# Optimization experiments

Hardware: AMD Instinct MI355X
Metric: run time of the kernel (lower is better)

The kernel has to match this reference:

```python
import jax, jax.numpy as jnp
import numpy as np
from jax import lax

NPOINT, RADIUS, NSAMPLE = 1024, 0.2, 32
MLP = [64, 64, 128]
EPS = 1e-5  # BatchNorm eps


def setup_inputs() -> dict:
    key = jax.random.key(0)
    ks = jax.random.split(key, 16)
    B, N, D = 16, 4096, 64
    inp = {
        "xyz": jax.random.uniform(ks[0], (B, 3, N), jnp.float32),   # points in unit cube
        "points": jax.random.normal(ks[1], (B, D, N), jnp.float32),  # per-point features
    }
    chans = [3 + D] + MLP  # grouped_xyz_norm (3) concat features (D)
    for i in range(3):
        ci, co = chans[i], chans[i + 1]
        inp[f"W{i}"] = jax.random.normal(ks[2 + 4 * i], (co, ci), jnp.float32) * (1.0 / np.sqrt(ci))
        inp[f"b{i}"] = jnp.zeros((co,), jnp.float32)
        inp[f"g{i}"] = jnp.ones((co,), jnp.float32)    # BN gamma
        inp[f"be{i}"] = jnp.zeros((co,), jnp.float32)  # BN beta
    return inp


def _fps(xyz, npoint):
    # xyz: [B,N,3] -> sampled indices [B,npoint]. Sequential farthest-point sampling.
    B, N, _ = xyz.shape

    def step(carry, _):
        distance, farthest = carry
        centroid = jnp.take_along_axis(xyz, farthest[:, None, None], axis=1)  # [B,1,3]
        d = jnp.sum((xyz - centroid) ** 2, -1)                                # [B,N]
        distance = jnp.minimum(distance, d)
        return (distance, jnp.argmax(distance, -1)), farthest

    init = (jnp.full((B, N), 1e10, xyz.dtype), jnp.zeros((B,), jnp.int32))
    _, idx = lax.scan(step, init, None, length=npoint)
    return idx.T  # [B, npoint]


def _index_points(pts, idx):
    # pts [B,N,C], idx [B,...] int -> [B,...,C]  (batched gather)
    return jax.vmap(lambda p, i: p[i])(pts, idx)


def _ball_query(radius, nsample, xyz, new_xyz):
    # xyz [B,N,3], new_xyz [B,S,3] -> group_idx [B,S,nsample]
    B, N, _ = xyz.shape
    sqr = (jnp.sum(new_xyz ** 2, -1)[:, :, None]
           + jnp.sum(xyz ** 2, -1)[:, None, :]
           - 2.0 * jnp.einsum('bsc,bnc->bsn', new_xyz, xyz))  # [B,S,N]
    # NB: source assigns N-1 (not N) to out-of-radius points; the == N fixup is a no-op,
    # kept here for faithfulness.
    gi = jnp.where(sqr > radius ** 2, N - 1, jnp.arange(N, dtype=jnp.int32)[None, None, :])
    gi = jnp.sort(gi, axis=-1)[:, :, :nsample]
    first = gi[:, :, :1]
    return jnp.where(gi == N, first, gi)


def _forward(xyz, points, params):
    xyzT = jnp.transpose(xyz, (0, 2, 1))    # [B,N,3]
    ptsT = jnp.transpose(points, (0, 2, 1))  # [B,N,D]
    B, N, _ = xyzT.shape
    fps_idx = _fps(xyzT, NPOINT)                              # [B,S]
    new_xyz = _index_points(xyzT, fps_idx)                    # [B,S,3]
    idx = _ball_query(RADIUS, NSAMPLE, xyzT, new_xyz)         # [B,S,K]
    grouped_xyz = _index_points(xyzT, idx) - new_xyz[:, :, None, :]  # [B,S,K,3]
    grouped_pts = _index_points(ptsT, idx)                    # [B,S,K,D]
    feat = jnp.concatenate([grouped_xyz, grouped_pts], -1)    # [B,S,K,3+D]
    x = jnp.transpose(feat, (0, 3, 2, 1))                     # [B,C,K,S]
    for (W, b, g, be) in params:
        x = jnp.einsum('bcks,oc->boks', x, W) + b[None, :, None, None]  # 1x1 conv
        mean = jnp.mean(x, axis=(0, 2, 3), keepdims=True)   # BN (training-mode batch stats)
        var = jnp.var(x, axis=(0, 2, 3), keepdims=True)
        x = (x - mean) / jnp.sqrt(var + EPS) * g[None, :, None, None] + be[None, :, None, None]
        x = jax.nn.relu(x)
    new_points = jnp.max(x, axis=2)                           # [B, mlp[-1], S]
    return jnp.transpose(new_xyz, (0, 2, 1)), new_points


def reference(xyz, points, W0, b0, g0, be0, W1, b1, g1, be1, W2, b2, g2, be2):
    params = [(W0, b0, g0, be0), (W1, b1, g1, be1), (W2, b2, g2, be2)]
    return _forward(xyz, points, params)
```

## Files before the change

### kernel.cpp

```cpp
#include <hip/hip_runtime.h>
#include <cstdint>
#include <cstddef>

#define BB 16
#define NN 4096
#define SS 1024
#define KK 32
#define MROWS (BB*SS*KK)
#define EPSV 1e-5f
#define OUT_OFF1 (BB*3*SS)

static constexpr size_t OFF_XYZT   = 0;
static constexpr size_t OFF_NEWXYZ = OFF_XYZT   + (size_t)BB*NN*16;
static constexpr size_t OFF_BALL   = OFF_NEWXYZ + (size_t)BB*SS*16;
static constexpr size_t OFF_STATS  = OFF_BALL   + (size_t)MROWS*4;
static constexpr size_t OFF_PROG   = OFF_STATS  + 2048;
static constexpr size_t OFF_PT     = OFF_PROG   + 256;
static constexpr size_t OFF_Y      = OFF_PT     + (size_t)BB*NN*64*4;
static constexpr size_t OFF_YMAX   = OFF_Y      + (size_t)MROWS*64*4;
static constexpr size_t OFF_YMIN   = OFF_YMAX   + (size_t)BB*SS*128*4;

__device__ __forceinline__ float sq3(float x, float y, float z) {
  return __fadd_rn(__fadd_rn(__fmul_rn(x,x), __fmul_rn(y,y)), __fmul_rn(z,z));
}

template<int CTRL>
__device__ __forceinline__ unsigned long long dpp_max_u64(unsigned long long k) {
  int lo = (int)(unsigned)k;
  int hi = (int)(unsigned)(k >> 32);
  unsigned olo = (unsigned)__builtin_amdgcn_update_dpp(0, lo, CTRL, 0xf, 0xf, true);
  unsigned ohi = (unsigned)__builtin_amdgcn_update_dpp(0, hi, CTRL, 0xf, 0xf, true);
  unsigned long long o = ((unsigned long long)ohi << 32) | (unsigned long long)olo;
  return o > k ? o : k;
}

__global__ __launch_bounds__(256) void trans_kernel(const float* __restrict__ xyz,
                                                    const float* __restrict__ pts,
                                                    float4* __restrict__ xyzt,
                                                    float* __restrict__ pt) {
  __shared__ float tl[64*65];
  int t = threadIdx.x;
  int k = blockIdx.x;
  int b = k >> 6, n0 = (k & 63) * 64;
  int ln = t & 63, hi = t >> 6;
#pragma unroll
  for (int i = 0; i < 16; ++i) {
    int c = 4*i + hi;
    tl[c*65 + ln] = pts[((size_t)b*64 + c)*NN + n0 + ln];
  }
  if (t < 64) {
    int n = n0 + t;
    const float* xb = xyz + (size_t)b*3*NN;
    xyzt[(size_t)b*NN + n] = make_float4(xb[n], xb[NN+n], xb[2*NN+n], 0.f);
  }
  __syncthreads();
#pragma unroll
  for (int i = 0; i < 16; ++i) {
    int nn = hi + 4*i;
    pt[((size_t)b*NN + n0 + nn)*64 + ln] = tl[ln*65 + nn];
  }
}

__global__ __launch_bounds__(256) void fps_ball_conv0(const float* __restrict__ xyz,
                                                      const float4* __restrict__ xyzt,
                                                      const float* __restrict__ pt,
                                                      float4* __restrict__ newxyz,
                                                      int* __restrict__ prog,
                                                      float* __restrict__ out,
                                                      const float* __restrict__ W0,
                                                      const float* __restrict__ bias0,
                                                      float* __restrict__ y,
                                                      float* __restrict__ stats0) {
  __shared__ __align__(16) char smem[65600];
  int t = threadIdx.x;

  if (blockIdx.x >= 16) {
    float4* Ws4  = (float4*)smem;
    float*  Ws   = (float*)Ws4;
    float4* Xs4  = (float4*)(smem + 17408);
    int*    bidx = (int*)(smem + 52224);
    int lane = t & 63, wv = t >> 6;
    int base = (blockIdx.x - 16)*4;
    int bs = base + wv;
    int b = bs >> 10;

    for (int idx = t; idx < 68*64; idx += 256) {
      int cc = idx >> 6, o = idx & 63;
      float v = 0.f;
      if (cc < 67) v = W0[o*67 + (cc < 64 ? cc+3 : cc-64)];
      Ws[(cc << 6) + o] = v;
    }

    int need = (base & (SS-1)) + 4;
    if (t == 0) {
      while (__hip_atomic_load(&prog[b], __ATOMIC_ACQUIRE, __HIP_MEMORY_SCOPE_AGENT) < need)
        __builtin_amdgcn_s_sleep(64);
    }
    __syncthreads();

    const float* xb = xyz + (size_t)b*3*NN;
    float4 c = newxyz[bs];
    float sumS = sq3(c.x, c.y, c.z);
    int count = 0;
    for (int ch = 0; ch < NN/64; ++ch) {
      int n = ch*64 + lane;
      float nx = xb[n], ny = xb[NN+n], nz = xb[2*NN+n];
      float sumN = sq3(nx, ny, nz);
      float dt   = __fadd_rn(__fadd_rn(__fmul_rn(c.x,nx), __fmul_rn(c.y,ny)), __fmul_rn(c.z,nz));
      float sqr  = __fsub_rn(__fadd_rn(sumS, sumN), __fmul_rn(2.0f, dt));
      bool isin = !(sqr > 0.04f);
      unsigned long long mask = __ballot(isin);
      int pos = count + (int)__popcll(mask & ((1ull << lane) - 1ull));
      if (isin && pos < KK) bidx[(wv << 5) + pos] = n;
      count += (int)__popcll(mask);
      if (count >= KK) break;
    }
    if (count < KK && lane >= count && lane < KK) bidx[(wv << 5) + lane] = NN-1;
    __syncthreads();

    {
      int rr = t >> 1, p = t & 1;
      int n = bidx[rr];
      const float4* src = (const float4*)(pt + ((size_t)(b*NN + n))*64) + 8*p;
#pragma unroll
      for (int jj = 0; jj < 8; ++jj) Xs4[rr*17 + 8*p + jj] = src[jj];
      if (p == 0) {
        float4 pz = xyzt[b*NN + n];
        float4 q  = newxyz[base + (rr >> 5)];
        float* X = (float*)Xs4;
        X[rr*68 + 64] = pz.x - q.x;
        X[rr*68 + 65] = pz.y - q.y;
        X[rr*68 + 66] = pz.z - q.z;
        X[rr*68 + 67] = 0.f;
      }
    }
    __syncthreads();

    int tc = t & 15, trs = (t >> 4) & 3;
    float accS[4], accQ[4];
#pragma unroll
    for (int j = 0; j < 4; ++j) { accS[j] = 0.f; accQ[j] = 0.f; }

    float acc[8][4];
#pragma unroll
    for (int i = 0; i < 8; ++i)
#pragma unroll
      for (int j = 0; j < 4; ++j) acc[i][j] = bias0[tc*4 + j];

    for (int c4 = 0; c4 < 17; ++c4) {
      float4 a[8];
#pragma unroll
      for (int i = 0; i < 8; ++i) a[i] = Xs4[(32*wv + trs + 4*i)*17 + c4];
      float4 w[4];
#pragma unroll
      for (int cc = 0; cc < 4; ++cc) w[cc] = Ws4[(4*c4 + cc)*16 + tc];
#pragma unroll
      for (int cc = 0; cc < 4; ++cc) {
#pragma unroll
        for (int i = 0; i < 8; ++i) {
          float av = (cc==0) ? a[i].x : (cc==1) ? a[i].y : (cc==2) ? a[i].z : a[i].w;
          acc[i][0] = fmaf(av, w[cc].x, acc[i][0]);
          acc[i][1] = fmaf(av, w[cc].y, acc[i][1]);
          acc[i][2] = fmaf(av, w[cc].z, acc[i][2]);
          acc[i][3] = fmaf(av, w[cc].w, acc[i][3]);
        }
      }
    }

#pragma unroll
    for (int i = 0; i < 8; ++i) {
      size_t rw = (size_t)base*32 + 32*wv + trs + 4*i;
      ((float4*)(y + rw*64))[tc] = make_float4(acc[i][0], acc[i][1], acc[i][2], acc[i][3]);
    }
#pragma unroll
    for (int i = 0; i < 8; ++i)
#pragma unroll
      for (int j = 0; j < 4; ++j) {
        float v = acc[i][j];
        accS[j] += v;
        accQ[j] = fmaf(v, v, accQ[j]);
      }

    __syncthreads();
    float* scratch = (float*)Xs4;
    if (t < 128) scratch[t] = 0.f;
    __syncthreads();
#pragma unroll
    for (int j = 0; j < 4; ++j) {
      atomicAdd(&scratch[tc*4 + j], accS[j]);
      atomicAdd(&scratch[64 + tc*4 + j], accQ[j]);
    }
    __syncthreads();
    if (t < 128) atomicAdd(&stats0[t], scratch[t]);
    return;
  }

  float4* sxyz = (float4*)smem;
  unsigned long long (*red)[4] = (unsigned long long (*)[4])(smem + 65536);
  int b = blockIdx.x;
  int lane = t & 63, wv = t >> 6;
  const float* xb = xyz + (size_t)b*3*NN;
  float px[16], py[16], pz[16], dd[16];
#pragma unroll
  for (int j = 0; j < 16; ++j) {
    int n = t + 256*j;
    px[j] = xb[n]; py[j] = xb[NN+n]; pz[j] = xb[2*NN+n];
    sxyz[n] = make_float4(px[j], py[j], pz[j], 0.f);
    dd[j] = 1e10f;
  }
  int f = 0;
  float mcx = 0.f, mcy = 0.f, mcz = 0.f;
  __syncthreads();
  for (int i = 0; i < SS; ++i) {
    float4 cc4 = sxyz[f];
    float cx = cc4.x, cy = cc4.y, cz = cc4.z;
    if (t == (i & 31)) { mcx = cx; mcy = cy; mcz = cz; }
    if ((i & 31) == 31) {
      if (t < 32) {
        int ci = i - 31 + t;
        newxyz[b*SS + ci] = make_float4(mcx, mcy, mcz, 0.f);
        out[(size_t)b*3*SS + ci]        = mcx;
        out[(size_t)b*3*SS + SS + ci]   = mcy;
        out[(size_t)b*3*SS + 2*SS + ci] = mcz;
      }
      if (t == 0)
        __hip_atomic_store(&prog[b], i+1, __ATOMIC_RELEASE, __HIP_MEMORY_SCOPE_AGENT);
    }
    if (i == SS-1) break;
    unsigned long long key[16];
#pragma unroll
    for (int j = 0; j < 16; ++j) {
      float dx = __fsub_rn(px[j], cx);
      float dy = __fsub_rn(py[j], cy);
      float dz = __fsub_rn(pz[j], cz);
      float d  = sq3(dx, dy, dz);
      float nd = dd[j] < d ? dd[j] : d;
      dd[j] = nd;
      key[j] = (((unsigned long long)__float_as_uint(nd)) << 32)
             | (unsigned)(NN-1 - (t + 256*j));
    }
#pragma unroll
    for (int w = 8; w >= 1; w >>= 1)
#pragma unroll
      for (int q = 0; q < w; ++q)
        key[q] = key[q] > key[q+w] ? key[q] : key[q+w];
    unsigned long long bk = key[0];
    bk = dpp_max_u64<0x111>(bk);
    bk = dpp_max_u64<0x112>(bk);
    bk = dpp_max_u64<0x114>(bk);
    bk = dpp_max_u64<0x118>(bk);
    bk = dpp_max_u64<0x142>(bk);
    bk = dpp_max_u64<0x143>(bk);
    if (lane == 63) red[i&1][wv] = bk;
    __syncthreads();
    unsigned long long best = red[i&1][0];
#pragma unroll
    for (int w = 1; w < 4; ++w) { unsigned long long v = red[i&1][w]; if (v > best) best = v; }
    f = (NN-1) - (int)(best & 0xffffffffull);
  }
}

template<int MODE, int CO>
__global__ __launch_bounds__(256) void conv_kernel(
    const float* xin, const float* __restrict__ W, const float* __restrict__ bias,
    const float* __restrict__ statsPrev, const float* __restrict__ gPrev,
    const float* __restrict__ bePrev, float* yout, float* __restrict__ statsOut,
    float* __restrict__ ymax, float* __restrict__ ymin) {
  constexpr int NC = CO/16;
  constexpr int CR = 64;
  constexpr int C4N = CR/4;
  __shared__ float4 Ws4[CR*CO/4];
  __shared__ float4 Xs4[128*17];
  __shared__ float scIn[64], shIn[64];
  float* Ws = (float*)Ws4;

  int t = threadIdx.x;
  int tc = t & 15;
  int wv = t >> 6;
  int trs = (t >> 4) & 3;
  if (t < 64) {
    float mean = statsPrev[t] * (1.0f/MROWS);
    float var  = statsPrev[64+t] * (1.0f/MROWS) - mean*mean;
    float inv  = 1.0f / sqrtf(var + EPSV);
    float sc   = gPrev[t] * inv;
    scIn[t] = sc; shIn[t] = bePrev[t] - mean*sc;
  }
  for (int idx = t; idx < CR*CO; idx += 256) {
    int cc = idx / CO, o = idx % CO;
    Ws[cc*CO + o] = W[o*64 + cc];
  }
  float bj[NC], accS[NC], accQ[NC];
#pragma unroll
  for (int j = 0; j < NC; ++j) { bj[j] = bias[tc*NC + j]; accS[j] = 0.f; accQ[j] = 0.f; }
  __syncthreads();

  for (int tile = blockIdx.x; tile < MROWS/128; tile += gridDim.x) {
    {
      const float4* src = (const float4*)(xin + (size_t)tile*128*64);
#pragma unroll
      for (int k = 0; k < 8; ++k) {
        int idx = t + 256*k;
        int row = idx >> 4, c4 = idx & 15;
        float4 v = src[idx];
        int c = 4*c4;
        v.x = fmaxf(0.f, fmaf(v.x, scIn[c+0], shIn[c+0]));
        v.y = fmaxf(0.f, fmaf(v.y, scIn[c+1], shIn[c+1]));
        v.z = fmaxf(0.f, fmaf(v.z, scIn[c+2], shIn[c+2]));
        v.w = fmaxf(0.f, fmaf(v.w, scIn[c+3], shIn[c+3]));
        Xs4[row*17 + c4] = v;
      }
    }
    __syncthreads();

    float acc[8][NC];
#pragma unroll
    for (int i = 0; i < 8; ++i)
#pragma unroll
      for (int j = 0; j < NC; ++j) acc[i][j] = bj[j];

    for (int c4 = 0; c4 < C4N; ++c4) {
      float4 a[8];
#pragma unroll
      for (int i = 0; i < 8; ++i) a[i] = Xs4[(32*wv + trs + 4*i)*17 + c4];
      float4 w[4][NC/4];
#pragma unroll
      for (int cc = 0; cc < 4; ++cc)
#pragma unroll
        for (int q = 0; q < NC/4; ++q)
          w[cc][q] = Ws4[(4*c4 + cc)*(CO/4) + tc*(NC/4) + q];
#pragma unroll
      for (int cc = 0; cc < 4; ++cc) {
#pragma unroll
        for (int i = 0; i < 8; ++i) {
          float av = (cc==0) ? a[i].x : (cc==1) ? a[i].y : (cc==2) ? a[i].z : a[i].w;
#pragma unroll
          for (int q = 0; q < NC/4; ++q) {
            acc[i][4*q+0] = fmaf(av, w[cc][q].x, acc[i][4*q+0]);
            acc[i][4*q+1] = fmaf(av, w[cc][q].y, acc[i][4*q+1]);
            acc[i][4*q+2] = fmaf(av, w[cc][q].z, acc[i][4*q+2]);
            acc[i][4*q+3] = fmaf(av, w[cc][q].w, acc[i][4*q+3]);
          }
        }
      }
    }

    if constexpr (MODE <= 1) {
#pragma unroll
      for (int i = 0; i < 8; ++i) {
        size_t rw = (size_t)tile*128 + 32*wv + trs + 4*i;
        float4 v = make_float4(acc[i][0], acc[i][1], acc[i][2], acc[i][3]);
        ((float4*)(yout + rw*64))[tc] = v;
      }
    }
#pragma unroll
    for (int i = 0; i < 8; ++i)
#pragma unroll
      for (int j = 0; j < NC; ++j) {
        float v = acc[i][j];
        accS[j] += v;
        accQ[j] = fmaf(v, v, accQ[j]);
      }

    if constexpr (MODE == 2) {
      float vmx[NC], vmn[NC];
#pragma unroll
      for (int j = 0; j < NC; ++j) {
        float mx = acc[0][j], mn = acc[0][j];
#pragma unroll
        for (int i = 1; i < 8; ++i) { mx = fmaxf(mx, acc[i][j]); mn = fminf(mn, acc[i][j]); }
        vmx[j] = mx; vmn[j] = mn;
      }
#pragma unroll
      for (int m = 16; m <= 32; m <<= 1)
#pragma unroll
        for (int j = 0; j < NC; ++j) {
          vmx[j] = fmaxf(vmx[j], __shfl_xor(vmx[j], m, 64));
          vmn[j] = fminf(vmn[j], __shfl_xor(vmn[j], m, 64));
        }
      if ((t & 63) < 16) {
        size_t gg = (size_t)tile*4 + wv;
        ((float4*)(ymax + gg*128 + 8*tc))[0] = make_float4(vmx[0], vmx[1], vmx[2], vmx[3]);
        ((float4*)(ymax + gg*128 + 8*tc))[1] = make_float4(vmx[4], vmx[5], vmx[6], vmx[7]);
        ((float4*)(ymin + gg*128 + 8*tc))[0] = make_float4(vmn[0], vmn[1], vmn[2], vmn[3]);
        ((float4*)(ymin + gg*128 + 8*tc))[1] = make_float4(vmn[4], vmn[5], vmn[6], vmn[7]);
      }
    }
    __syncthreads();
  }

  float* scratch = (float*)Xs4;
  if (t < 2*CO) scratch[t] = 0.f;
  __syncthreads();
#pragma unroll
  for (int j = 0; j < NC; ++j) {
    atomicAdd(&scratch[tc*NC + j], accS[j]);
    atomicAdd(&scratch[CO + tc*NC + j], accQ[j]);
  }
  __syncthreads();
  if (t < 2*CO) atomicAdd(&statsOut[t], scratch[t]);
}

__global__ __launch_bounds__(256) void final_kernel(const float4* __restrict__ ymax4,
                                                    const float4* __restrict__ ymin4,
                                                    const float* __restrict__ stats2,
                                                    const float* __restrict__ g2,
                                                    const float* __restrict__ be2,
                                                    float* __restrict__ out) {
  __shared__ float sc3[128], sh3[128];
  __shared__ float tile[64*129];
  int t = threadIdx.x;
  if (t < 128) {
    float mean = stats2[t] * (1.0f/MROWS);
    float var  = stats2[128+t] * (1.0f/MROWS) - mean*mean;
    float sc   = g2[t] / sqrtf(var + EPSV);
    sc3[t] = sc; sh3[t] = be2[t] - mean*sc;
  }
  __syncthreads();
  int b = blockIdx.x, s0 = blockIdx.y*64;
#pragma unroll
  for (int pass = 0; pass < 8; ++pass) {
    int srow = pass*8 + (t >> 5);
    int o4 = (t & 31)*4;
    size_t base = (size_t)(b*SS + s0 + srow)*32 + (t & 31);
    float4 vx = ymax4[base], vn = ymin4[base];
#pragma unroll
    for (int e = 0; e < 4; ++e) {
      int o = o4 + e;
      float sc = sc3[o];
      float v = sc > 0.f ? ((const float*)&vx)[e] : ((const float*)&vn)[e];
      tile[srow*129 + o] = fmaxf(0.f, fmaf(v, sc, sh3[o]));
    }
  }
  __syncthreads();
  int s = t & 63;
  size_t obase = (size_t)OUT_OFF1 + (size_t)b*128*SS + s0 + s;
#pragma unroll
  for (int oi = 0; oi < 32; ++oi) {
    int o = (t >> 6) + 4*oi;
    out[obase + (size_t)o*SS] = tile[s*129 + o];
  }
}

extern "C" void kernel_launch(void* const* d_in, const int* in_sizes, int n_in,
                              void* d_out, int out_size, void* d_ws, size_t ws_size,
                              hipStream_t stream) {
  const float* xyz = (const float*)d_in[0];
  const float* pts = (const float*)d_in[1];
  const float* W0  = (const float*)d_in[2];
  const float* b0  = (const float*)d_in[3];
  const float* g0  = (const float*)d_in[4];
  const float* be0 = (const float*)d_in[5];
  const float* W1  = (const float*)d_in[6];
  const float* b1  = (const float*)d_in[7];
  const float* g1  = (const float*)d_in[8];
  const float* be1 = (const float*)d_in[9];
  const float* W2  = (const float*)d_in[10];
  const float* b2  = (const float*)d_in[11];
  const float* g2  = (const float*)d_in[12];
  const float* be2 = (const float*)d_in[13];
  float* out = (float*)d_out;
  char* ws = (char*)d_ws;

  float4* xyzt   = (float4*)(ws + OFF_XYZT);
  float4* newxyz = (float4*)(ws + OFF_NEWXYZ);
  float*  stats  = (float*)(ws + OFF_STATS);
  int*    prog   = (int*)(ws + OFF_PROG);
  float*  pt     = (float*)(ws + OFF_PT);
  float*  y      = (float*)(ws + OFF_Y);
  float*  ymax   = (float*)(ws + OFF_YMAX);
  float*  ymin   = (float*)(ws + OFF_YMIN);

  hipMemsetAsync(stats, 0, 2048 + 256, stream);
  trans_kernel<<<BB*(NN/64), 256, 0, stream>>>(xyz, pts, xyzt, pt);
  fps_ball_conv0<<<16 + BB*SS/4, 256, 0, stream>>>(
      xyz, (const float4*)xyzt, pt, newxyz, prog, out, W0, b0, y, stats);
  conv_kernel<1,64><<<1024, 256, 0, stream>>>(y, W1, b1,
      stats, g0, be0, y, stats+128, nullptr, nullptr);
  conv_kernel<2,128><<<1024, 256, 0, stream>>>(y, W2, b2,
      stats+128, g1, be1, nullptr, stats+256, ymax, ymin);
  final_kernel<<<dim3(BB, SS/64), 256, 0, stream>>>((const float4*)ymax, (const float4*)ymin,
      stats+256, g2, be2, out);
}
```

Baseline: 1.154 ms.

## Read conv input tiles directly from global instead of staging through LDS

The 1x1-conv kernels no longer copy each 128-row input tile into shared memory. Each thread now loads its float4 input values straight from global memory inside the channel loop and applies the previous layer's BN+ReLU in registers. This removes the per-tile staging pass and its two barriers, and shrinks shared memory use, which may allow more resident blocks; the grid is doubled to 2048 blocks to use that. The cost is that the 16 lanes sharing a row now re-read the same addresses through the vector cache instead of LDS, and the loads are strided rather than coalesced, so the kernels lean more heavily on L1/L2 bandwidth.

```diff
diff --git a/kernel.cpp b/kernel.cpp
--- a/kernel.cpp
+++ b/kernel.cpp
@@ -267,11 +267,9 @@
     const float* __restrict__ bePrev, float* yout, float* __restrict__ statsOut,
     float* __restrict__ ymax, float* __restrict__ ymin) {
   constexpr int NC = CO/16;
-  constexpr int CR = 64;
-  constexpr int C4N = CR/4;
-  __shared__ float4 Ws4[CR*CO/4];
-  __shared__ float4 Xs4[128*17];
+  __shared__ float4 Ws4[64*CO/4];
   __shared__ float scIn[64], shIn[64];
+  __shared__ float scratch[2*CO];
   float* Ws = (float*)Ws4;
 
   int t = threadIdx.x;
@@ -285,7 +283,7 @@
     float sc   = gPrev[t] * inv;
     scIn[t] = sc; shIn[t] = bePrev[t] - mean*sc;
   }
-  for (int idx = t; idx < CR*CO; idx += 256) {
+  for (int idx = t; idx < 64*CO; idx += 256) {
     int cc = idx / CO, o = idx % CO;
     Ws[cc*CO + o] = W[o*64 + cc];
   }
@@ -295,22 +293,7 @@
   __syncthreads();
 
   for (int tile = blockIdx.x; tile < MROWS/128; tile += gridDim.x) {
-    {
-      const float4* src = (const float4*)(xin + (size_t)tile*128*64);
-#pragma unroll
-      for (int k = 0; k < 8; ++k) {
-        int idx = t + 256*k;
-        int row = idx >> 4, c4 = idx & 15;
-        float4 v = src[idx];
-        int c = 4*c4;
-        v.x = fmaxf(0.f, fmaf(v.x, scIn[c+0], shIn[c+0]));
-        v.y = fmaxf(0.f, fmaf(v.y, scIn[c+1], shIn[c+1]));
-        v.z = fmaxf(0.f, fmaf(v.z, scIn[c+2], shIn[c+2]));
-        v.w = fmaxf(0.f, fmaf(v.w, scIn[c+3], shIn[c+3]));
-        Xs4[row*17 + c4] = v;
-      }
-    }
-    __syncthreads();
+    const float4* src = (const float4*)(xin + (size_t)tile*128*64);
 
     float acc[8][NC];
 #pragma unroll
@@ -318,10 +301,19 @@
 #pragma unroll
       for (int j = 0; j < NC; ++j) acc[i][j] = bj[j];
 
-    for (int c4 = 0; c4 < C4N; ++c4) {
+    for (int c4 = 0; c4 < 16; ++c4) {
       float4 a[8];
 #pragma unroll
-      for (int i = 0; i < 8; ++i) a[i] = Xs4[(32*wv + trs + 4*i)*17 + c4];
+      for (int i = 0; i < 8; ++i) a[i] = src[(size_t)(32*wv + trs + 4*i)*16 + c4];
+      float4 sc4 = ((const float4*)scIn)[c4];
+      float4 sh4 = ((const float4*)shIn)[c4];
+#pragma unroll
+      for (int i = 0; i < 8; ++i) {
+        a[i].x = fmaxf(0.f, fmaf(a[i].x, sc4.x, sh4.x));
+        a[i].y = fmaxf(0.f, fmaf(a[i].y, sc4.y, sh4.y));
+        a[i].z = fmaxf(0.f, fmaf(a[i].z, sc4.z, sh4.z));
+        a[i].w = fmaxf(0.f, fmaf(a[i].w, sc4.w, sh4.w));
+      }
       float4 w[4][NC/4];
 #pragma unroll
       for (int cc = 0; cc < 4; ++cc)
@@ -385,10 +377,9 @@
         ((float4*)(ymin + gg*128 + 8*tc))[1] = make_float4(vmn[4], vmn[5], vmn[6], vmn[7]);
       }
     }
-    __syncthreads();
-  }
-
-  float* scratch = (float*)Xs4;
+  }
+
+  __syncthreads();
   if (t < 2*CO) scratch[t] = 0.f;
   __syncthreads();
 #pragma unroll
@@ -474,9 +465,9 @@
   trans_kernel<<<BB*(NN/64), 256, 0, stream>>>(xyz, pts, xyzt, pt);
   fps_ball_conv0<<<16 + BB*SS/4, 256, 0, stream>>>(
       xyz, (const float4*)xyzt, pt, newxyz, prog, out, W0, b0, y, stats);
-  conv_kernel<1,64><<<1024, 256, 0, stream>>>(y, W1, b1,
+  conv_kernel<1,64><<<2048, 256, 0, stream>>>(y, W1, b1,
       stats, g0, be0, y, stats+128, nullptr, nullptr);
-  conv_kernel<2,128><<<1024, 256, 0, stream>>>(y, W2, b2,
+  conv_kernel<2,128><<<2048, 256, 0, stream>>>(y, W2, b2,
       stats+128, g1, be1, nullptr, stats+256, ymax, ymin);
   final_kernel<<<dim3(BB, SS/64), 256, 0, stream>>>((const float4*)ymax, (const float4*)ymin,
       stats+256, g2, be2, out);
```

Result: slower. 1.253 ms (+8.6%).
